# Kernel optimization log

Hardware: AMD Instinct MI355X
Metric: run time of the kernel (lower is better)

Reference implementation:

```python
import jax, jax.numpy as jnp
import numpy as np

N = 50000
E = 800000
IN_FEAT = 128
HIDDEN = 64
HEADS = 4
CLASSES = 40
NEG_SLOPE = 0.2


def setup_inputs() -> dict:
    key = jax.random.key(0)
    ks = jax.random.split(key, 12)
    x = jax.random.normal(ks[0], (N, IN_FEAT), dtype=jnp.float32)
    # edge_index without self loops (module removes then re-adds them)
    src = jax.random.randint(ks[1], (E,), 0, N)
    off = jax.random.randint(ks[2], (E,), 1, N)
    dst = (src + off) % N  # guaranteed dst != src
    edge_index = jnp.stack([src, dst]).astype(jnp.int64)
    g = 1.0 / np.sqrt(IN_FEAT)
    lin1_w = jax.random.normal(ks[3], (IN_FEAT, HEADS * HIDDEN), dtype=jnp.float32) * g
    lin1_b = jax.random.normal(ks[4], (HEADS * HIDDEN,), dtype=jnp.float32) * 0.01
    att1 = jax.random.normal(ks[5], (1, HEADS, 2 * HIDDEN), dtype=jnp.float32) * (1.0 / np.sqrt(2 * HIDDEN))
    bias1 = jnp.zeros((HEADS * HIDDEN,), dtype=jnp.float32)
    lin2_w = jax.random.normal(ks[6], (HEADS * HIDDEN, CLASSES), dtype=jnp.float32) * (1.0 / np.sqrt(HEADS * HIDDEN))
    lin2_b = jax.random.normal(ks[7], (CLASSES,), dtype=jnp.float32) * 0.01
    att2 = jax.random.normal(ks[8], (1, 1, 2 * CLASSES), dtype=jnp.float32) * (1.0 / np.sqrt(2 * CLASSES))
    bias2 = jnp.zeros((CLASSES,), dtype=jnp.float32)
    return {"x": x, "edge_index": edge_index, "lin1_w": lin1_w, "lin1_b": lin1_b,
            "att1": att1, "bias1": bias1, "lin2_w": lin2_w, "lin2_b": lin2_b,
            "att2": att2, "bias2": bias2}


def gat_conv(x, src, dst, W, b_lin, att, bias, heads, oc):
    n = x.shape[0]
    fea = (x @ W + b_lin).reshape(n, heads, oc)            # [N, H, C]
    # attention logits: (cat([x_i, x_j]) * att).sum(-1) decomposed per node
    score_i = jnp.einsum('nhc,hc->nh', fea, att[0, :, :oc])  # target half
    score_j = jnp.einsum('nhc,hc->nh', fea, att[0, :, oc:])  # source half
    alpha = score_i[dst] + score_j[src]                    # [E, H]
    alpha = jax.nn.leaky_relu(alpha, NEG_SLOPE)
    # segment softmax over target node
    amax = jax.ops.segment_max(alpha, dst, num_segments=n)
    alpha = jnp.exp(alpha - amax[dst])
    asum = jax.ops.segment_sum(alpha, dst, num_segments=n)
    alpha = alpha / (asum[dst] + 1e-16)
    # message = x_j * alpha; scatter-add to target
    msg = fea[src] * alpha[:, :, None]                     # [E, H, C]
    out = jax.ops.segment_sum(msg, dst, num_segments=n)
    return out.reshape(n, heads * oc) + bias               # concat=True


def reference(x, edge_index, lin1_w, lin1_b, att1, bias1, lin2_w, lin2_b, att2, bias2):
    n = x.shape[0]
    loop = jnp.arange(n, dtype=edge_index.dtype)
    src = jnp.concatenate([edge_index[0], loop])  # add self loops
    dst = jnp.concatenate([edge_index[1], loop])
    h = gat_conv(x, src, dst, lin1_w, lin1_b, att1, bias1, HEADS, HIDDEN)
    h = jax.nn.relu(h)
    h = gat_conv(h, src, dst, lin2_w, lin2_b, att2, bias2, 1, CLASSES)
    return jax.nn.softmax(h, axis=1)
```

## Files before the change

kernel.cpp:

```cpp
#include <hip/hip_runtime.h>
#include <hip/hip_fp16.h>

#define NN 50000
#define NE 800000
#define INFEAT 128
#define F1 256
#define HID 64
#define CLS 40
#define NEGS 0.2f
#define NB 49

__device__ __forceinline__ float lrelu(float x) { return x > 0.0f ? x : NEGS * x; }

struct alignas(8) H4 { __half2 a, b; };

#define BM 128
#define BN 64
#define BK 32
__global__ __launch_bounds__(256) void gemm1_k(const float* __restrict__ A,
                                               const float* __restrict__ W,
                                               const float* __restrict__ b,
                                               const float* __restrict__ att1,
                                               __half* __restrict__ feah,
                                               float* __restrict__ sI,
                                               float* __restrict__ sJ) {
    __shared__ float As[BK][BM + 4];
    __shared__ float Bs[BK][BN];
    int tid = threadIdx.x;
    int row0 = blockIdx.x * BM;
    int head = blockIdx.y;
    int col0 = head * BN;
    int tx = tid & 15, ty = tid >> 4;
    float acc[8][4] = {};
    for (int k0 = 0; k0 < INFEAT; k0 += BK) {
        {
            int r = tid >> 3;
            int c = (tid & 7) * 4;
            #pragma unroll
            for (int rr = r; rr < BM; rr += 32) {
                int grow = row0 + rr;
                float4 v = make_float4(0.f, 0.f, 0.f, 0.f);
                if (grow < NN) v = *(const float4*)&A[(size_t)grow * INFEAT + k0 + c];
                As[c + 0][rr] = v.x; As[c + 1][rr] = v.y;
                As[c + 2][rr] = v.z; As[c + 3][rr] = v.w;
            }
        }
        {
            int r = tid >> 4;
            int c = (tid & 15) * 4;
            #pragma unroll
            for (int rr = r; rr < BK; rr += 16)
                *(float4*)&Bs[rr][c] = *(const float4*)&W[(size_t)(k0 + rr) * F1 + col0 + c];
        }
        __syncthreads();
        #pragma unroll
        for (int k = 0; k < BK; ++k) {
            float4 a0 = *(const float4*)&As[k][ty * 8];
            float4 a1 = *(const float4*)&As[k][ty * 8 + 4];
            float4 bv = *(const float4*)&Bs[k][tx * 4];
            float a[8] = {a0.x, a0.y, a0.z, a0.w, a1.x, a1.y, a1.z, a1.w};
            float bb[4] = {bv.x, bv.y, bv.z, bv.w};
            #pragma unroll
            for (int i = 0; i < 8; ++i)
                #pragma unroll
                for (int j = 0; j < 4; ++j) acc[i][j] += a[i] * bb[j];
        }
        __syncthreads();
    }
    int gcol = col0 + tx * 4;
    float4 bv = *(const float4*)&b[gcol];
    float aI0 = att1[head * 2 * HID + tx * 4 + 0];
    float aI1 = att1[head * 2 * HID + tx * 4 + 1];
    float aI2 = att1[head * 2 * HID + tx * 4 + 2];
    float aI3 = att1[head * 2 * HID + tx * 4 + 3];
    float aJ0 = att1[head * 2 * HID + HID + tx * 4 + 0];
    float aJ1 = att1[head * 2 * HID + HID + tx * 4 + 1];
    float aJ2 = att1[head * 2 * HID + HID + tx * 4 + 2];
    float aJ3 = att1[head * 2 * HID + HID + tx * 4 + 3];
    float sIp[8], sJp[8];
    #pragma unroll
    for (int i = 0; i < 8; ++i) {
        float4 o = make_float4(acc[i][0] + bv.x, acc[i][1] + bv.y,
                               acc[i][2] + bv.z, acc[i][3] + bv.w);
        int grow = row0 + ty * 8 + i;
        if (grow < NN) {
            H4 v;
            v.a = __floats2half2_rn(o.x, o.y);
            v.b = __floats2half2_rn(o.z, o.w);
            *(H4*)&feah[(size_t)grow * F1 + gcol] = v;
        }
        sIp[i] = o.x * aI0 + o.y * aI1 + o.z * aI2 + o.w * aI3;
        sJp[i] = o.x * aJ0 + o.y * aJ1 + o.z * aJ2 + o.w * aJ3;
    }
    #pragma unroll
    for (int off = 1; off < 16; off <<= 1) {
        #pragma unroll
        for (int i = 0; i < 8; ++i) {
            sIp[i] += __shfl_xor(sIp[i], off);
            sJp[i] += __shfl_xor(sJp[i], off);
        }
    }
    if (tx == 0) {
        #pragma unroll
        for (int i = 0; i < 8; ++i) {
            int grow = row0 + ty * 8 + i;
            if (grow < NN) {
                sI[grow * 4 + head] = sIp[i];
                sJ[grow * 4 + head] = sJp[i];
            }
        }
    }
}

__global__ void hist_k(const int* __restrict__ dst, int* __restrict__ deg,
                       int* __restrict__ ord) {
    int e = blockIdx.x * blockDim.x + threadIdx.x;
    if (e < NE) ord[e] = atomicAdd(&deg[dst[e]], 1);
}

__global__ __launch_bounds__(1024) void scan1_k(const int* __restrict__ deg,
                                                int* __restrict__ row_off,
                                                int* __restrict__ bsum) {
    __shared__ int tmp[1024];
    int tid = threadIdx.x;
    int gid = blockIdx.x * 1024 + tid;
    int v = (gid < NN) ? deg[gid] : 0;
    tmp[tid] = v;
    __syncthreads();
    #pragma unroll
    for (int off = 1; off < 1024; off <<= 1) {
        int t = (tid >= off) ? tmp[tid - off] : 0;
        __syncthreads();
        tmp[tid] += t;
        __syncthreads();
    }
    if (gid < NN) row_off[gid] = tmp[tid] - v;
    if (tid == 1023) bsum[blockIdx.x] = tmp[1023];
}

__global__ void scan2_k(const int* __restrict__ bsum, int* __restrict__ bpref) {
    int tid = threadIdx.x;
    int orig = (tid < NB) ? bsum[tid] : 0;
    int v = orig;
    #pragma unroll
    for (int off = 1; off < 64; off <<= 1) {
        int t = __shfl_up(v, off);
        if (tid >= off) v += t;
    }
    if (tid < NB) bpref[tid] = v - orig;
}

__global__ __launch_bounds__(1024) void scan3_k(int* __restrict__ row_off,
                                                const int* __restrict__ bpref) {
    int gid = blockIdx.x * 1024 + threadIdx.x;
    if (gid < NN) row_off[gid] += bpref[blockIdx.x];
    if (gid == 0) row_off[NN] = NE;
}

__global__ void scatter_k(const int* __restrict__ src, const int* __restrict__ dst,
                          const int* __restrict__ ord, const int* __restrict__ row_off,
                          const float* __restrict__ sI, const float* __restrict__ sJ,
                          int* __restrict__ csr, float4* __restrict__ ep4) {
    int e = blockIdx.x * blockDim.x + threadIdx.x;
    if (e >= NE) return;
    int s = src[e], d = dst[e];
    int pos = row_off[d] + ord[e];
    float4 si = *(const float4*)&sI[d * 4];
    float4 sj = *(const float4*)&sJ[s * 4];
    float4 r;
    r.x = __expf(lrelu(si.x + sj.x));
    r.y = __expf(lrelu(si.y + sj.y));
    r.z = __expf(lrelu(si.z + sj.z));
    r.w = __expf(lrelu(si.w + sj.w));
    csr[pos] = s;
    ep4[pos] = r;
}

__global__ __launch_bounds__(256, 6) void agg1_k(const __half* __restrict__ feah,
                                                 const float* __restrict__ sI,
                                                 const float* __restrict__ sJ,
                                                 const float* __restrict__ epf,
                                                 const int* __restrict__ row_off,
                                                 const int* __restrict__ csr,
                                                 const float* __restrict__ bias,
                                                 float* __restrict__ out) {
    int wid = threadIdx.x >> 6, lane = threadIdx.x & 63;
    int n = blockIdx.x * 4 + wid;
    if (n >= NN) return;
    int h = lane >> 4;
    int c = lane * 4;
    float p = __expf(lrelu(sI[n * 4 + h] + sJ[n * 4 + h]));
    float asum = p;
    H4 vs = *(const H4*)&feah[(size_t)n * F1 + c];
    float2 sx = __half22float2(vs.a), sy = __half22float2(vs.b);
    float4 acc = make_float4(sx.x * p, sx.y * p, sy.x * p, sy.y * p);
    int beg = row_off[n], end = row_off[n + 1];
    int e = beg;
    for (; e + 8 <= end; e += 8) {
        int s0 = csr[e + 0], s1 = csr[e + 1], s2 = csr[e + 2], s3 = csr[e + 3];
        int s4 = csr[e + 4], s5 = csr[e + 5], s6 = csr[e + 6], s7 = csr[e + 7];
        float p0 = epf[(e + 0) * 4 + h], p1 = epf[(e + 1) * 4 + h];
        float p2 = epf[(e + 2) * 4 + h], p3 = epf[(e + 3) * 4 + h];
        float p4 = epf[(e + 4) * 4 + h], p5 = epf[(e + 5) * 4 + h];
        float p6 = epf[(e + 6) * 4 + h], p7 = epf[(e + 7) * 4 + h];
        H4 v0 = *(const H4*)&feah[(size_t)s0 * F1 + c];
        H4 v1 = *(const H4*)&feah[(size_t)s1 * F1 + c];
        H4 v2 = *(const H4*)&feah[(size_t)s2 * F1 + c];
        H4 v3 = *(const H4*)&feah[(size_t)s3 * F1 + c];
        H4 v4 = *(const H4*)&feah[(size_t)s4 * F1 + c];
        H4 v5 = *(const H4*)&feah[(size_t)s5 * F1 + c];
        H4 v6 = *(const H4*)&feah[(size_t)s6 * F1 + c];
        H4 v7 = *(const H4*)&feah[(size_t)s7 * F1 + c];
        asum += ((p0 + p1) + (p2 + p3)) + ((p4 + p5) + (p6 + p7));
        float2 x0 = __half22float2(v0.a), y0 = __half22float2(v0.b);
        float2 x1 = __half22float2(v1.a), y1 = __half22float2(v1.b);
        float2 x2 = __half22float2(v2.a), y2 = __half22float2(v2.b);
        float2 x3 = __half22float2(v3.a), y3 = __half22float2(v3.b);
        float2 x4 = __half22float2(v4.a), y4 = __half22float2(v4.b);
        float2 x5 = __half22float2(v5.a), y5 = __half22float2(v5.b);
        float2 x6 = __half22float2(v6.a), y6 = __half22float2(v6.b);
        float2 x7 = __half22float2(v7.a), y7 = __half22float2(v7.b);
        acc.x += (x0.x * p0 + x1.x * p1 + x2.x * p2 + x3.x * p3)
               + (x4.x * p4 + x5.x * p5 + x6.x * p6 + x7.x * p7);
        acc.y += (x0.y * p0 + x1.y * p1 + x2.y * p2 + x3.y * p3)
               + (x4.y * p4 + x5.y * p5 + x6.y * p6 + x7.y * p7);
        acc.z += (y0.x * p0 + y1.x * p1 + y2.x * p2 + y3.x * p3)
               + (y4.x * p4 + y5.x * p5 + y6.x * p6 + y7.x * p7);
        acc.w += (y0.y * p0 + y1.y * p1 + y2.y * p2 + y3.y * p3)
               + (y4.y * p4 + y5.y * p5 + y6.y * p6 + y7.y * p7);
    }
    for (; e + 4 <= end; e += 4) {
        int s0 = csr[e], s1 = csr[e + 1], s2 = csr[e + 2], s3 = csr[e + 3];
        float p0 = epf[(e + 0) * 4 + h], p1 = epf[(e + 1) * 4 + h];
        float p2 = epf[(e + 2) * 4 + h], p3 = epf[(e + 3) * 4 + h];
        H4 v0 = *(const H4*)&feah[(size_t)s0 * F1 + c];
        H4 v1 = *(const H4*)&feah[(size_t)s1 * F1 + c];
        H4 v2 = *(const H4*)&feah[(size_t)s2 * F1 + c];
        H4 v3 = *(const H4*)&feah[(size_t)s3 * F1 + c];
        asum += (p0 + p1) + (p2 + p3);
        float2 x0 = __half22float2(v0.a), y0 = __half22float2(v0.b);
        float2 x1 = __half22float2(v1.a), y1 = __half22float2(v1.b);
        float2 x2 = __half22float2(v2.a), y2 = __half22float2(v2.b);
        float2 x3 = __half22float2(v3.a), y3 = __half22float2(v3.b);
        acc.x += x0.x * p0 + x1.x * p1 + x2.x * p2 + x3.x * p3;
        acc.y += x0.y * p0 + x1.y * p1 + x2.y * p2 + x3.y * p3;
        acc.z += y0.x * p0 + y1.x * p1 + y2.x * p2 + y3.x * p3;
        acc.w += y0.y * p0 + y1.y * p1 + y2.y * p2 + y3.y * p3;
    }
    for (; e < end; ++e) {
        int s = csr[e];
        float pe = epf[e * 4 + h];
        asum += pe;
        H4 v = *(const H4*)&feah[(size_t)s * F1 + c];
        float2 x = __half22float2(v.a), y = __half22float2(v.b);
        acc.x += x.x * pe; acc.y += x.y * pe;
        acc.z += y.x * pe; acc.w += y.y * pe;
    }
    float inv = 1.0f / (asum + 1e-16f);
    float4 bv = *(const float4*)&bias[c];
    float4 o;
    o.x = fmaxf(acc.x * inv + bv.x, 0.f);
    o.y = fmaxf(acc.y * inv + bv.y, 0.f);
    o.z = fmaxf(acc.z * inv + bv.z, 0.f);
    o.w = fmaxf(acc.w * inv + bv.w, 0.f);
    *(float4*)&out[(size_t)n * F1 + c] = o;
}

#define G2N 102
__global__ __launch_bounds__(256) void gemm2_k(const float* __restrict__ h1,
                                               const float* __restrict__ W2,
                                               const float* __restrict__ b2,
                                               const float* __restrict__ att2,
                                               float* __restrict__ fea2,
                                               float* __restrict__ s2I,
                                               float* __restrict__ s2J) {
    __shared__ float Ws[F1 * CLS];
    __shared__ float redI[G2N][5];
    __shared__ float redJ[G2N][5];
    int tid = threadIdx.x;
    for (int i = tid * 4; i < F1 * CLS; i += 256 * 4)
        *(float4*)&Ws[i] = *(const float4*)&W2[i];
    __syncthreads();
    int nl = tid / 5, g = tid - nl * 5;
    int na = blockIdx.x * G2N + nl * 2;
    int nb = na + 1;
    bool actA = (tid < 255) && (na < NN);
    bool actB = (tid < 255) && (nb < NN);
    int c0 = g * 8;
    float accA[8] = {}, accB[8] = {};
    if (actA) {
        const float* rowA = h1 + (size_t)na * F1;
        const float* rowB = h1 + (size_t)(actB ? nb : na) * F1;
        for (int k = 0; k < F1; k += 4) {
            float4 ha = *(const float4*)&rowA[k];
            float4 hb = *(const float4*)&rowB[k];
            float a[4] = {ha.x, ha.y, ha.z, ha.w};
            float bl[4] = {hb.x, hb.y, hb.z, hb.w};
            #pragma unroll
            for (int kk = 0; kk < 4; ++kk) {
                float4 w0 = *(const float4*)&Ws[(k + kk) * CLS + c0];
                float4 w1 = *(const float4*)&Ws[(k + kk) * CLS + c0 + 4];
                accA[0] += a[kk] * w0.x; accA[1] += a[kk] * w0.y;
                accA[2] += a[kk] * w0.z; accA[3] += a[kk] * w0.w;
                accA[4] += a[kk] * w1.x; accA[5] += a[kk] * w1.y;
                accA[6] += a[kk] * w1.z; accA[7] += a[kk] * w1.w;
                accB[0] += bl[kk] * w0.x; accB[1] += bl[kk] * w0.y;
                accB[2] += bl[kk] * w0.z; accB[3] += bl[kk] * w0.w;
                accB[4] += bl[kk] * w1.x; accB[5] += bl[kk] * w1.y;
                accB[6] += bl[kk] * w1.z; accB[7] += bl[kk] * w1.w;
            }
        }
        float4 bb0 = *(const float4*)&b2[c0];
        float4 bb1 = *(const float4*)&b2[c0 + 4];
        float bias8[8] = {bb0.x, bb0.y, bb0.z, bb0.w, bb1.x, bb1.y, bb1.z, bb1.w};
        float sIa = 0.f, sJa = 0.f, sIb = 0.f, sJb = 0.f;
        #pragma unroll
        for (int j = 0; j < 8; ++j) {
            accA[j] += bias8[j];
            accB[j] += bias8[j];
            float aI = att2[c0 + j], aJ = att2[CLS + c0 + j];
            sIa += accA[j] * aI; sJa += accA[j] * aJ;
            sIb += accB[j] * aI; sJb += accB[j] * aJ;
        }
        *(float4*)&fea2[(size_t)na * CLS + c0]     = make_float4(accA[0], accA[1], accA[2], accA[3]);
        *(float4*)&fea2[(size_t)na * CLS + c0 + 4] = make_float4(accA[4], accA[5], accA[6], accA[7]);
        redI[nl * 2][g] = sIa;
        redJ[nl * 2][g] = sJa;
        if (actB) {
            *(float4*)&fea2[(size_t)nb * CLS + c0]     = make_float4(accB[0], accB[1], accB[2], accB[3]);
            *(float4*)&fea2[(size_t)nb * CLS + c0 + 4] = make_float4(accB[4], accB[5], accB[6], accB[7]);
            redI[nl * 2 + 1][g] = sIb;
            redJ[nl * 2 + 1][g] = sJb;
        }
    }
    __syncthreads();
    if (actA && g == 0) {
        int r = nl * 2;
        s2I[na] = redI[r][0] + redI[r][1] + redI[r][2] + redI[r][3] + redI[r][4];
        s2J[na] = redJ[r][0] + redJ[r][1] + redJ[r][2] + redJ[r][3] + redJ[r][4];
        if (actB) {
            s2I[nb] = redI[r + 1][0] + redI[r + 1][1] + redI[r + 1][2] + redI[r + 1][3] + redI[r + 1][4];
            s2J[nb] = redJ[r + 1][0] + redJ[r + 1][1] + redJ[r + 1][2] + redJ[r + 1][3] + redJ[r + 1][4];
        }
    }
}

__global__ __launch_bounds__(256) void agg2_k(const float* __restrict__ fea2,
                                              const float* __restrict__ s2I,
                                              const float* __restrict__ s2J,
                                              const int* __restrict__ row_off,
                                              const int* __restrict__ csr,
                                              const float* __restrict__ bias2,
                                              float* __restrict__ out) {
    int wid = threadIdx.x >> 6, lane = threadIdx.x & 63;
    int n = blockIdx.x * 4 + wid;
    if (n >= NN) return;
    float si = s2I[n], sjn = s2J[n];
    int c = lane < CLS ? lane : 0;
    float p = __expf(lrelu(si + sjn));
    float asum = p;
    float acc = fea2[(size_t)n * CLS + c] * p;
    int beg = row_off[n], end = row_off[n + 1];
    int e = beg;
    for (; e + 8 <= end; e += 8) {
        int s0 = csr[e + 0], s1 = csr[e + 1], s2 = csr[e + 2], s3 = csr[e + 3];
        int s4 = csr[e + 4], s5 = csr[e + 5], s6 = csr[e + 6], s7 = csr[e + 7];
        float a0 = s2J[s0], a1 = s2J[s1], a2 = s2J[s2], a3 = s2J[s3];
        float a4 = s2J[s4], a5 = s2J[s5], a6 = s2J[s6], a7 = s2J[s7];
        float f0 = fea2[(size_t)s0 * CLS + c];
        float f1 = fea2[(size_t)s1 * CLS + c];
        float f2 = fea2[(size_t)s2 * CLS + c];
        float f3 = fea2[(size_t)s3 * CLS + c];
        float f4 = fea2[(size_t)s4 * CLS + c];
        float f5 = fea2[(size_t)s5 * CLS + c];
        float f6 = fea2[(size_t)s6 * CLS + c];
        float f7 = fea2[(size_t)s7 * CLS + c];
        float p0 = __expf(lrelu(si + a0));
        float p1 = __expf(lrelu(si + a1));
        float p2 = __expf(lrelu(si + a2));
        float p3 = __expf(lrelu(si + a3));
        float p4 = __expf(lrelu(si + a4));
        float p5 = __expf(lrelu(si + a5));
        float p6 = __expf(lrelu(si + a6));
        float p7 = __expf(lrelu(si + a7));
        asum += ((p0 + p1) + (p2 + p3)) + ((p4 + p5) + (p6 + p7));
        acc += (f0 * p0 + f1 * p1 + f2 * p2 + f3 * p3)
             + (f4 * p4 + f5 * p5 + f6 * p6 + f7 * p7);
    }
    for (; e + 4 <= end; e += 4) {
        int s0 = csr[e], s1 = csr[e + 1], s2 = csr[e + 2], s3 = csr[e + 3];
        float p0 = __expf(lrelu(si + s2J[s0]));
        float p1 = __expf(lrelu(si + s2J[s1]));
        float p2 = __expf(lrelu(si + s2J[s2]));
        float p3 = __expf(lrelu(si + s2J[s3]));
        float f0 = fea2[(size_t)s0 * CLS + c];
        float f1 = fea2[(size_t)s1 * CLS + c];
        float f2 = fea2[(size_t)s2 * CLS + c];
        float f3 = fea2[(size_t)s3 * CLS + c];
        asum += (p0 + p1) + (p2 + p3);
        acc += f0 * p0 + f1 * p1 + f2 * p2 + f3 * p3;
    }
    for (; e < end; ++e) {
        int s = csr[e];
        float pe = __expf(lrelu(si + s2J[s]));
        asum += pe;
        acc += fea2[(size_t)s * CLS + c] * pe;
    }
    float row = acc / (asum + 1e-16f) + bias2[c];
    float v = (lane < CLS) ? row : -3.0e38f;
    float vm = v;
    #pragma unroll
    for (int off = 32; off; off >>= 1) vm = fmaxf(vm, __shfl_xor(vm, off));
    float ex = (lane < CLS) ? __expf(v - vm) : 0.f;
    float es = ex;
    #pragma unroll
    for (int off = 32; off; off >>= 1) es += __shfl_xor(es, off);
    if (lane < CLS) out[(size_t)n * CLS + lane] = ex / es;
}

extern "C" void kernel_launch(void* const* d_in, const int* in_sizes, int n_in,
                              void* d_out, int out_size, void* d_ws, size_t ws_size,
                              hipStream_t stream) {
    const float* x     = (const float*)d_in[0];
    const int*   ei    = (const int*)d_in[1];
    const float* w1    = (const float*)d_in[2];
    const float* b1    = (const float*)d_in[3];
    const float* att1  = (const float*)d_in[4];
    const float* bias1 = (const float*)d_in[5];
    const float* w2    = (const float*)d_in[6];
    const float* b2    = (const float*)d_in[7];
    const float* att2  = (const float*)d_in[8];
    const float* bias2 = (const float*)d_in[9];
    const int* src = ei;
    const int* dst = ei + NE;
    float* out = (float*)d_out;

    char* p = (char*)d_ws;
    auto alloc = [&](size_t bytes) {
        char* r = p;
        p += (bytes + 255) & ~(size_t)255;
        return r;
    };
    __half* fea1h = (__half*)alloc((size_t)NN * F1 * 2);
    float* h1     = (float*)alloc((size_t)NN * F1 * 4);
    float* sI1    = (float*)alloc((size_t)NN * 4 * 4);
    float* sJ1    = (float*)alloc((size_t)NN * 4 * 4);
    float* fea2   = (float*)alloc((size_t)NN * CLS * 4);
    float* s2I    = (float*)alloc((size_t)NN * 4);
    float* s2J    = (float*)alloc((size_t)NN * 4);
    int*   deg    = (int*)alloc((size_t)NN * 4);
    int*   row_off= (int*)alloc((size_t)(NN + 1) * 4);
    int*   bsum   = (int*)alloc((size_t)NB * 4);
    int*   bpref  = (int*)alloc((size_t)NB * 4);
    int*   ord    = (int*)alloc((size_t)NE * 4);
    int*   csr    = (int*)alloc((size_t)NE * 4);
    float* ep1    = (float*)alloc((size_t)NE * 4 * 4);

    hipMemsetAsync(deg, 0, (size_t)NN * 4, stream);

    dim3 g1((NN + BM - 1) / BM, F1 / BN);
    gemm1_k<<<g1, 256, 0, stream>>>(x, w1, b1, att1, fea1h, sI1, sJ1);
    hist_k<<<(NE + 255) / 256, 256, 0, stream>>>(dst, deg, ord);
    scan1_k<<<NB, 1024, 0, stream>>>(deg, row_off, bsum);
    scan2_k<<<1, 64, 0, stream>>>(bsum, bpref);
    scan3_k<<<NB, 1024, 0, stream>>>(row_off, bpref);
    scatter_k<<<(NE + 255) / 256, 256, 0, stream>>>(src, dst, ord, row_off,
                                                    sI1, sJ1, csr, (float4*)ep1);
    agg1_k<<<(NN + 3) / 4, 256, 0, stream>>>(fea1h, sI1, sJ1, ep1, row_off, csr, bias1, h1);
    gemm2_k<<<(NN + G2N - 1) / G2N, 256, 0, stream>>>(h1, w2, b2, att2, fea2, s2I, s2J);
    agg2_k<<<(NN + 3) / 4, 256, 0, stream>>>(fea2, s2I, s2J, row_off, csr, bias2, out);
}
```

Before: 258.3 us.

## Store layer-2 features in fp16 and register-prefetch next GEMM1 tile

```diff
diff --git a/kernel.cpp b/kernel.cpp
--- a/kernel.cpp
+++ b/kernel.cpp
@@ -13,6 +13,7 @@
 __device__ __forceinline__ float lrelu(float x) { return x > 0.0f ? x : NEGS * x; }
 
 struct alignas(8) H4 { __half2 a, b; };
+struct alignas(16) H8 { __half2 a, b, c, d; };
 
 #define BM 128
 #define BN 64
@@ -31,28 +32,36 @@
     int head = blockIdx.y;
     int col0 = head * BN;
     int tx = tid & 15, ty = tid >> 4;
+    int ar = tid >> 3;
+    int ac = (tid & 7) * 4;
+    int br = tid >> 4;
+    int bc = (tid & 15) * 4;
+    float4 pa[4], pb[2];
+    auto load_tile = [&](int k0) {
+        #pragma unroll
+        for (int i = 0; i < 4; ++i) {
+            int grow = row0 + ar + i * 32;
+            pa[i] = (grow < NN) ? *(const float4*)&A[(size_t)grow * INFEAT + k0 + ac]
+                                : make_float4(0.f, 0.f, 0.f, 0.f);
+        }
+        #pragma unroll
+        for (int i = 0; i < 2; ++i)
+            pb[i] = *(const float4*)&W[(size_t)(k0 + br + i * 16) * F1 + col0 + bc];
+    };
     float acc[8][4] = {};
+    load_tile(0);
     for (int k0 = 0; k0 < INFEAT; k0 += BK) {
-        {
-            int r = tid >> 3;
-            int c = (tid & 7) * 4;
-            #pragma unroll
-            for (int rr = r; rr < BM; rr += 32) {
-                int grow = row0 + rr;
-                float4 v = make_float4(0.f, 0.f, 0.f, 0.f);
-                if (grow < NN) v = *(const float4*)&A[(size_t)grow * INFEAT + k0 + c];
-                As[c + 0][rr] = v.x; As[c + 1][rr] = v.y;
-                As[c + 2][rr] = v.z; As[c + 3][rr] = v.w;
-            }
-        }
-        {
-            int r = tid >> 4;
-            int c = (tid & 15) * 4;
-            #pragma unroll
-            for (int rr = r; rr < BK; rr += 16)
-                *(float4*)&Bs[rr][c] = *(const float4*)&W[(size_t)(k0 + rr) * F1 + col0 + c];
-        }
+        #pragma unroll
+        for (int i = 0; i < 4; ++i) {
+            int rr = ar + i * 32;
+            As[ac + 0][rr] = pa[i].x; As[ac + 1][rr] = pa[i].y;
+            As[ac + 2][rr] = pa[i].z; As[ac + 3][rr] = pa[i].w;
+        }
+        #pragma unroll
+        for (int i = 0; i < 2; ++i)
+            *(float4*)&Bs[br + i * 16][bc] = pb[i];
         __syncthreads();
+        if (k0 + BK < INFEAT) load_tile(k0 + BK);
         #pragma unroll
         for (int k = 0; k < BK; ++k) {
             float4 a0 = *(const float4*)&As[k][ty * 8];
@@ -271,7 +280,7 @@
                                                const float* __restrict__ W2,
                                                const float* __restrict__ b2,
                                                const float* __restrict__ att2,
-                                               float* __restrict__ fea2,
+                                               __half* __restrict__ fea2h,
                                                float* __restrict__ s2I,
                                                float* __restrict__ s2J) {
     __shared__ float Ws[F1 * CLS];
@@ -322,13 +331,21 @@
             sIa += accA[j] * aI; sJa += accA[j] * aJ;
             sIb += accB[j] * aI; sJb += accB[j] * aJ;
         }
-        *(float4*)&fea2[(size_t)na * CLS + c0]     = make_float4(accA[0], accA[1], accA[2], accA[3]);
-        *(float4*)&fea2[(size_t)na * CLS + c0 + 4] = make_float4(accA[4], accA[5], accA[6], accA[7]);
+        H8 ha8;
+        ha8.a = __floats2half2_rn(accA[0], accA[1]);
+        ha8.b = __floats2half2_rn(accA[2], accA[3]);
+        ha8.c = __floats2half2_rn(accA[4], accA[5]);
+        ha8.d = __floats2half2_rn(accA[6], accA[7]);
+        *(H8*)&fea2h[(size_t)na * CLS + c0] = ha8;
         redI[nl * 2][g] = sIa;
         redJ[nl * 2][g] = sJa;
         if (actB) {
-            *(float4*)&fea2[(size_t)nb * CLS + c0]     = make_float4(accB[0], accB[1], accB[2], accB[3]);
-            *(float4*)&fea2[(size_t)nb * CLS + c0 + 4] = make_float4(accB[4], accB[5], accB[6], accB[7]);
+            H8 hb8;
+            hb8.a = __floats2half2_rn(accB[0], accB[1]);
+            hb8.b = __floats2half2_rn(accB[2], accB[3]);
+            hb8.c = __floats2half2_rn(accB[4], accB[5]);
+            hb8.d = __floats2half2_rn(accB[6], accB[7]);
+            *(H8*)&fea2h[(size_t)nb * CLS + c0] = hb8;
             redI[nl * 2 + 1][g] = sIb;
             redJ[nl * 2 + 1][g] = sJb;
         }
@@ -345,7 +362,7 @@
     }
 }
 
-__global__ __launch_bounds__(256) void agg2_k(const float* __restrict__ fea2,
+__global__ __launch_bounds__(256) void agg2_k(const __half* __restrict__ fea2h,
                                               const float* __restrict__ s2I,
                                               const float* __restrict__ s2J,
                                               const int* __restrict__ row_off,
@@ -359,7 +376,7 @@
     int c = lane < CLS ? lane : 0;
     float p = __expf(lrelu(si + sjn));
     float asum = p;
-    float acc = fea2[(size_t)n * CLS + c] * p;
+    float acc = __half2float(fea2h[(size_t)n * CLS + c]) * p;
     int beg = row_off[n], end = row_off[n + 1];
     int e = beg;
     for (; e + 8 <= end; e += 8) {
@@ -367,14 +384,14 @@
         int s4 = csr[e + 4], s5 = csr[e + 5], s6 = csr[e + 6], s7 = csr[e + 7];
         float a0 = s2J[s0], a1 = s2J[s1], a2 = s2J[s2], a3 = s2J[s3];
         float a4 = s2J[s4], a5 = s2J[s5], a6 = s2J[s6], a7 = s2J[s7];
-        float f0 = fea2[(size_t)s0 * CLS + c];
-        float f1 = fea2[(size_t)s1 * CLS + c];
-        float f2 = fea2[(size_t)s2 * CLS + c];
-        float f3 = fea2[(size_t)s3 * CLS + c];
-        float f4 = fea2[(size_t)s4 * CLS + c];
-        float f5 = fea2[(size_t)s5 * CLS + c];
-        float f6 = fea2[(size_t)s6 * CLS + c];
-        float f7 = fea2[(size_t)s7 * CLS + c];
+        __half f0 = fea2h[(size_t)s0 * CLS + c];
+        __half f1 = fea2h[(size_t)s1 * CLS + c];
+        __half f2 = fea2h[(size_t)s2 * CLS + c];
+        __half f3 = fea2h[(size_t)s3 * CLS + c];
+        __half f4 = fea2h[(size_t)s4 * CLS + c];
+        __half f5 = fea2h[(size_t)s5 * CLS + c];
+        __half f6 = fea2h[(size_t)s6 * CLS + c];
+        __half f7 = fea2h[(size_t)s7 * CLS + c];
         float p0 = __expf(lrelu(si + a0));
         float p1 = __expf(lrelu(si + a1));
         float p2 = __expf(lrelu(si + a2));
@@ -384,8 +401,10 @@
         float p6 = __expf(lrelu(si + a6));
         float p7 = __expf(lrelu(si + a7));
         asum += ((p0 + p1) + (p2 + p3)) + ((p4 + p5) + (p6 + p7));
-        acc += (f0 * p0 + f1 * p1 + f2 * p2 + f3 * p3)
-             + (f4 * p4 + f5 * p5 + f6 * p6 + f7 * p7);
+        acc += (__half2float(f0) * p0 + __half2float(f1) * p1
+              + __half2float(f2) * p2 + __half2float(f3) * p3)
+             + (__half2float(f4) * p4 + __half2float(f5) * p5
+              + __half2float(f6) * p6 + __half2float(f7) * p7);
     }
     for (; e + 4 <= end; e += 4) {
         int s0 = csr[e], s1 = csr[e + 1], s2 = csr[e + 2], s3 = csr[e + 3];
@@ -393,18 +412,19 @@
         float p1 = __expf(lrelu(si + s2J[s1]));
         float p2 = __expf(lrelu(si + s2J[s2]));
         float p3 = __expf(lrelu(si + s2J[s3]));
-        float f0 = fea2[(size_t)s0 * CLS + c];
-        float f1 = fea2[(size_t)s1 * CLS + c];
-        float f2 = fea2[(size_t)s2 * CLS + c];
-        float f3 = fea2[(size_t)s3 * CLS + c];
+        __half f0 = fea2h[(size_t)s0 * CLS + c];
+        __half f1 = fea2h[(size_t)s1 * CLS + c];
+        __half f2 = fea2h[(size_t)s2 * CLS + c];
+        __half f3 = fea2h[(size_t)s3 * CLS + c];
         asum += (p0 + p1) + (p2 + p3);
-        acc += f0 * p0 + f1 * p1 + f2 * p2 + f3 * p3;
+        acc += __half2float(f0) * p0 + __half2float(f1) * p1
+             + __half2float(f2) * p2 + __half2float(f3) * p3;
     }
     for (; e < end; ++e) {
         int s = csr[e];
         float pe = __expf(lrelu(si + s2J[s]));
         asum += pe;
-        acc += fea2[(size_t)s * CLS + c] * pe;
+        acc += __half2float(fea2h[(size_t)s * CLS + c]) * pe;
     }
     float row = acc / (asum + 1e-16f) + bias2[c];
     float v = (lane < CLS) ? row : -3.0e38f;
@@ -445,7 +465,7 @@
     float* h1     = (float*)alloc((size_t)NN * F1 * 4);
     float* sI1    = (float*)alloc((size_t)NN * 4 * 4);
     float* sJ1    = (float*)alloc((size_t)NN * 4 * 4);
-    float* fea2   = (float*)alloc((size_t)NN * CLS * 4);
+    __half* fea2h = (__half*)alloc((size_t)NN * CLS * 2);
     float* s2I    = (float*)alloc((size_t)NN * 4);
     float* s2J    = (float*)alloc((size_t)NN * 4);
     int*   deg    = (int*)alloc((size_t)NN * 4);
@@ -467,6 +487,6 @@
     scatter_k<<<(NE + 255) / 256, 256, 0, stream>>>(src, dst, ord, row_off,
                                                     sI1, sJ1, csr, (float4*)ep1);
     agg1_k<<<(NN + 3) / 4, 256, 0, stream>>>(fea1h, sI1, sJ1, ep1, row_off, csr, bias1, h1);
-    gemm2_k<<<(NN + G2N - 1) / G2N, 256, 0, stream>>>(h1, w2, b2, att2, fea2, s2I, s2J);
-    agg2_k<<<(NN + 3) / 4, 256, 0, stream>>>(fea2, s2I, s2J, row_off, csr, bias2, out);
-}
+    gemm2_k<<<(NN + G2N - 1) / G2N, 256, 0, stream>>>(h1, w2, b2, att2, fea2h, s2I, s2J);
+    agg2_k<<<(NN + 3) / 4, 256, 0, stream>>>(fea2h, s2I, s2J, row_off, csr, bias2, out);
+}
```

New measurement: 257.9 us. Within noise of the previous version (-0.2%).
